# Kernel optimization log

Measured on AMD Instinct MI355X. Metric: run time of the kernel, lower is better.

The kernel has to match this reference:

```python
import jax, jax.numpy as jnp
import numpy as np

N_HEADS = 16
NEG_INF = -1e30  # stand-in for -inf, safe in fp32/bf16


def setup_inputs() -> dict:
    key = jax.random.key(0)
    k1, k2, k3, k4 = jax.random.split(key, 4)
    B, T, C = 8, 1024, 1024
    x = jax.random.normal(k1, (B, T, C), dtype=jnp.float32)
    # torch nn.Linear weight layout: [out_features, in_features]
    w_attn = jax.random.normal(k2, (3 * C, C), dtype=jnp.float32) * 0.02
    w_proj = jax.random.normal(k3, (C, C), dtype=jnp.float32) * 0.02
    b_proj = jax.random.normal(k4, (C,), dtype=jnp.float32) * 0.02
    return {"x": x, "w_attn": w_attn, "w_proj": w_proj, "b_proj": b_proj}


def reference(x, w_attn, w_proj, b_proj):
    B, T, C = x.shape
    H = N_HEADS
    d = C // H
    # fused QKV projection (bias=False); source splits as keys, queries, values
    qkv = x @ w_attn.T  # [B, T, 3C]
    k, q, v = jnp.split(qkv, 3, axis=-1)
    # [B, T, C] -> [B, H, T, d]
    k = k.reshape(B, T, H, d).transpose(0, 2, 1, 3)
    q = q.reshape(B, T, H, d).transpose(0, 2, 1, 3)
    v = v.reshape(B, T, H, d).transpose(0, 2, 1, 3)
    scale = 1.0 / jnp.sqrt(jnp.asarray(d, dtype=x.dtype))
    att = jnp.einsum('bhqd,bhkd->bhqk', q, k) * scale  # [B, H, T, T]
    causal = jnp.tril(jnp.ones((T, T), dtype=bool))
    att = jnp.where(causal, att, NEG_INF)
    att = jax.nn.softmax(att, axis=-1)
    y = jnp.einsum('bhqk,bhkd->bhqd', att, v)  # [B, H, T, d]
    y = y.transpose(0, 2, 1, 3).reshape(B, T, C)
    return y @ w_proj.T + b_proj
```

## Files before the change

### kernel.cpp

```cpp
#include <hip/hip_runtime.h>
#include <stdint.h>

typedef unsigned short u16;
typedef __attribute__((ext_vector_type(8))) short short8;
typedef __attribute__((ext_vector_type(4))) float f32x4;

__device__ __forceinline__ float bf2f(u16 u) {
    union { unsigned u; float f; } x; x.u = ((unsigned)u) << 16; return x.f;
}
__device__ __forceinline__ float bf_lo(unsigned w) {
    union { unsigned u; float f; } x; x.u = w << 16; return x.f;
}
__device__ __forceinline__ float bf_hi(unsigned w) {
    union { unsigned u; float f; } x; x.u = w & 0xffff0000u; return x.f;
}
__device__ __forceinline__ u16 f2bf(float f) {
    union { float f; unsigned u; } x; x.f = f;
    unsigned r = x.u + 0x7fffu + ((x.u >> 16) & 1u);
    return (u16)(r >> 16);
}
__device__ __forceinline__ uint4 cvt8(const float* p) {
    float4 a = *reinterpret_cast<const float4*>(p);
    float4 b = *reinterpret_cast<const float4*>(p + 4);
    uint4 r;
    r.x = (unsigned)f2bf(a.x) | ((unsigned)f2bf(a.y) << 16);
    r.y = (unsigned)f2bf(a.z) | ((unsigned)f2bf(a.w) << 16);
    r.z = (unsigned)f2bf(b.x) | ((unsigned)f2bf(b.y) << 16);
    r.w = (unsigned)f2bf(b.z) | ((unsigned)f2bf(b.w) << 16);
    return r;
}

__device__ __forceinline__ void gl16(const u16* g, u16* l) {
    __builtin_amdgcn_global_load_lds(
        (const __attribute__((address_space(1))) void*)g,
        (__attribute__((address_space(3))) void*)l, 16, 0, 0);
}

__global__ __launch_bounds__(256) void cvt_kernel(const float* __restrict__ in,
                                                  u16* __restrict__ out, int n8) {
    int i = blockIdx.x * 256 + threadIdx.x;
    if (i < n8) *reinterpret_cast<uint4*>(&out[(size_t)i * 8]) = cvt8(&in[(size_t)i * 8]);
}

__global__ __launch_bounds__(256) void cvt3_kernel(const float* __restrict__ a, int na8,
                                                   const float* __restrict__ b, int nb8,
                                                   const float* __restrict__ c, int nc8,
                                                   u16* __restrict__ dst) {
    int i = blockIdx.x * 256 + threadIdx.x;
    const float* src; int off;
    if (i < na8)            { src = a; off = i; }
    else if (i < na8 + nb8) { src = b; off = i - na8; }
    else if (i < na8 + nb8 + nc8) { src = c; off = i - na8 - nb8; }
    else return;
    *reinterpret_cast<uint4*>(&dst[(size_t)i * 8]) = cvt8(&src[(size_t)off * 8]);
}

#define BM 128
#define BN 128
#define BK 32
#define BKA 64

template<bool CF32>
__global__ __launch_bounds__(256) void gemm_bt_a(const u16* __restrict__ A,
                                                 const u16* __restrict__ W,
                                                 void* __restrict__ Cv,
                                                 const float* __restrict__ bias,
                                                 int M, int N, int K, int lda,
                                                 u16* __restrict__ vt) {
    __shared__ __align__(16) u16 As[2][BM * BKA];
    __shared__ __align__(16) u16 Ws[2][BN * BKA];

    const int tid  = threadIdx.x;
    const int lane = tid & 63;
    const int w    = tid >> 6;
    const int wr   = w >> 1;
    const int wc   = w & 1;
    const int quad = lane >> 4;
    const int l16  = lane & 15;

    const int row0 = blockIdx.y * BM;
    const int col0 = blockIdx.x * BN;

    const int srow = w * 8 + (lane >> 3);
    const int gc   = (lane & 7) ^ (lane >> 3);

    const u16* gA[4]; const u16* gW[4];
#pragma unroll
    for (int p = 0; p < 4; p++) {
        gA[p] = A + (size_t)(row0 + p * 32 + srow) * lda + gc * 8;
        gW[p] = W + (size_t)(col0 + p * 32 + srow) * K  + gc * 8;
    }
    const int lofs = (w * 8) * BKA;

    const int cr0 = (quad ^ (l16 & 7)) * 8;

    f32x4 acc[4][4] = {};

#pragma unroll
    for (int p = 0; p < 4; p++) {
        gl16(gA[p], &As[0][p * 32 * BKA + lofs]);
        gl16(gW[p], &Ws[0][p * 32 * BKA + lofs]);
    }

    int cur = 0;
    for (int k0 = 0; k0 < K; k0 += BKA) {
        __syncthreads();
        if (k0 + BKA < K) {
            const int nxt = cur ^ 1;
#pragma unroll
            for (int p = 0; p < 4; p++) {
                gl16(gA[p] + k0 + BKA, &As[nxt][p * 32 * BKA + lofs]);
                gl16(gW[p] + k0 + BKA, &Ws[nxt][p * 32 * BKA + lofs]);
            }
        }

#pragma unroll
        for (int ks = 0; ks < 2; ks++) {
            const int cc = cr0 ^ (ks * 32);
            short8 af[4], bfr[4];
#pragma unroll
            for (int i = 0; i < 4; i++)
                af[i] = *reinterpret_cast<const short8*>(&As[cur][(wr * 64 + i * 16 + l16) * BKA + cc]);
#pragma unroll
            for (int j = 0; j < 4; j++)
                bfr[j] = *reinterpret_cast<const short8*>(&Ws[cur][(wc * 64 + j * 16 + l16) * BKA + cc]);
#pragma unroll
            for (int i = 0; i < 4; i++)
#pragma unroll
                for (int j = 0; j < 4; j++)
                    acc[i][j] = __builtin_amdgcn_mfma_f32_16x16x32_bf16(af[i], bfr[j], acc[i][j], 0, 0, 0);
        }
        cur ^= 1;
    }

    if (vt != nullptr && col0 >= 2048) {
        const int b = row0 >> 10;
#pragma unroll
        for (int j = 0; j < 4; j++) {
            const int hd = col0 - 2048 + wc * 64 + j * 16 + l16;
            u16* dstc = vt + (size_t)(b * 1024 + hd) * 1024 + (row0 & 1023) + wr * 64;
#pragma unroll
            for (int i = 0; i < 4; i++) {
                const int t0 = i * 16 + quad * 4;
                u16 pk[4];
#pragma unroll
                for (int r = 0; r < 4; r++) pk[r] = f2bf(acc[i][j][r]);
                *reinterpret_cast<uint2*>(dstc + t0) = *reinterpret_cast<uint2*>(pk);
            }
        }
    } else {
#pragma unroll
        for (int j = 0; j < 4; j++) {
            const int col = col0 + wc * 64 + j * 16 + l16;
            const float bval = bias ? bias[col] : 0.0f;
#pragma unroll
            for (int i = 0; i < 4; i++) {
#pragma unroll
                for (int r = 0; r < 4; r++) {
                    const int row = row0 + wr * 64 + i * 16 + quad * 4 + r;
                    if (CF32) ((float*)Cv)[(size_t)row * N + col] = acc[i][j][r] + bval;
                    else      ((u16*)Cv)[(size_t)row * N + col]  = f2bf(acc[i][j][r] + bval);
                }
            }
        }
    }
}

template<bool AF32, bool WF32, bool CF32>
__global__ __launch_bounds__(256) void gemm_bt(const void* __restrict__ Av,
                                               const void* __restrict__ Wv,
                                               void* __restrict__ Cv,
                                               const float* __restrict__ bias,
                                               int M, int N, int K, int lda) {
    __shared__ __align__(16) u16 As[BM * BK];
    __shared__ __align__(16) u16 Ws[BN * BK];

    const int tid  = threadIdx.x;
    const int lane = tid & 63;
    const int wave = tid >> 6;
    const int wr   = wave >> 1;
    const int wc   = wave & 1;
    const int quad = lane >> 4;
    const int l16  = lane & 15;

    const int row0 = blockIdx.y * BM;
    const int col0 = blockIdx.x * BN;

    const int sr = tid >> 2;
    const int sc = (tid & 3) * 8;

    f32x4 acc[4][4] = {};

    for (int k0 = 0; k0 < K; k0 += BK) {
        __syncthreads();
        if (AF32) {
            const float* A = (const float*)Av;
            *reinterpret_cast<uint4*>(&As[(sr)      * BK + sc]) = cvt8(&A[(size_t)(row0 + sr)      * lda + k0 + sc]);
            *reinterpret_cast<uint4*>(&As[(sr + 64) * BK + sc]) = cvt8(&A[(size_t)(row0 + sr + 64) * lda + k0 + sc]);
        } else {
            const u16* A = (const u16*)Av;
            *reinterpret_cast<uint4*>(&As[(sr)      * BK + sc]) =
                *reinterpret_cast<const uint4*>(&A[(size_t)(row0 + sr)      * lda + k0 + sc]);
            *reinterpret_cast<uint4*>(&As[(sr + 64) * BK + sc]) =
                *reinterpret_cast<const uint4*>(&A[(size_t)(row0 + sr + 64) * lda + k0 + sc]);
        }
        if (WF32) {
            const float* W = (const float*)Wv;
            *reinterpret_cast<uint4*>(&Ws[(sr)      * BK + sc]) = cvt8(&W[(size_t)(col0 + sr)      * K + k0 + sc]);
            *reinterpret_cast<uint4*>(&Ws[(sr + 64) * BK + sc]) = cvt8(&W[(size_t)(col0 + sr + 64) * K + k0 + sc]);
        } else {
            const u16* W = (const u16*)Wv;
            *reinterpret_cast<uint4*>(&Ws[(sr)      * BK + sc]) =
                *reinterpret_cast<const uint4*>(&W[(size_t)(col0 + sr)      * K + k0 + sc]);
            *reinterpret_cast<uint4*>(&Ws[(sr + 64) * BK + sc]) =
                *reinterpret_cast<const uint4*>(&W[(size_t)(col0 + sr + 64) * K + k0 + sc]);
        }
        __syncthreads();

        short8 af[4], bfr[4];
#pragma unroll
        for (int i = 0; i < 4; i++)
            af[i] = *reinterpret_cast<const short8*>(&As[(wr * 64 + i * 16 + l16) * BK + quad * 8]);
#pragma unroll
        for (int j = 0; j < 4; j++)
            bfr[j] = *reinterpret_cast<const short8*>(&Ws[(wc * 64 + j * 16 + l16) * BK + quad * 8]);

#pragma unroll
        for (int i = 0; i < 4; i++)
#pragma unroll
            for (int j = 0; j < 4; j++)
                acc[i][j] = __builtin_amdgcn_mfma_f32_16x16x32_bf16(af[i], bfr[j], acc[i][j], 0, 0, 0);
    }

#pragma unroll
    for (int j = 0; j < 4; j++) {
        const int col = col0 + wc * 64 + j * 16 + l16;
        const float bval = bias ? bias[col] : 0.0f;
#pragma unroll
        for (int i = 0; i < 4; i++) {
#pragma unroll
            for (int r = 0; r < 4; r++) {
                const int row = row0 + wr * 64 + i * 16 + quad * 4 + r;
                if (CF32) ((float*)Cv)[(size_t)row * N + col] = acc[i][j][r] + bval;
                else      ((u16*)Cv)[(size_t)row * N + col]  = f2bf(acc[i][j][r] + bval);
            }
        }
    }
}

__global__ __launch_bounds__(256) void vtrans_kernel(const u16* __restrict__ qkv,
                                                     u16* __restrict__ vt) {
    const int bid = blockIdx.x;
    const int tt = bid & 15, h = (bid >> 4) & 15, b = bid >> 8;
    const int t0 = tt * 64;
    __shared__ __align__(16) u16 tile[64 * 72];
    const int tr = threadIdx.x >> 2, tc = (threadIdx.x & 3) * 16;
    const u16* src = qkv + (size_t)(b * 1024 + t0 + tr) * 3072 + 2048 + h * 64 + tc;
    *reinterpret_cast<uint4*>(&tile[tr * 72 + tc])     = *reinterpret_cast<const uint4*>(src);
    *reinterpret_cast<uint4*>(&tile[tr * 72 + tc + 8]) = *reinterpret_cast<const uint4*>(src + 8);
    __syncthreads();
    const int dh = tr, t1 = tc;
    __align__(16) u16 buf[16];
#pragma unroll
    for (int i = 0; i < 16; i++) buf[i] = tile[(t1 + i) * 72 + dh];
    u16* dst = vt + ((size_t)(b * 16 + h) * 64 + dh) * 1024 + t0 + t1;
    *reinterpret_cast<uint4*>(dst)     = *reinterpret_cast<uint4*>(&buf[0]);
    *reinterpret_cast<uint4*>(dst + 8) = *reinterpret_cast<uint4*>(&buf[8]);
}

#define SK 72

__global__ __launch_bounds__(256) void fattn_kernel(u16* __restrict__ qkv,
                                                    const u16* __restrict__ vt) {
    __shared__ __align__(16) u16 Ks[64 * SK];
    __shared__ __align__(16) u16 Vs[64 * SK];
    __shared__ __align__(16) u16 Ps[4][32 * SK];
    __shared__ __align__(16) float aS[4][32];

    const int tid  = threadIdx.x;
    const int lane = tid & 63;
    const int w    = tid >> 6;
    const int quad = lane >> 4;
    const int l16  = lane & 15;

    const int bid = blockIdx.x;
    const int qt  = 7 - (bid >> 7);
    const int bh  = bid & 127;
    const int b   = bh >> 4;
    const int h   = bh & 15;

    u16* qb        = qkv + (size_t)b * 1024 * 3072;
    const u16* vtb = vt + (size_t)bh * 64 * 1024;

    const int qrow0 = qt * 128 + w * 32;

    short8 qf[2][2];
#pragma unroll
    for (int mj = 0; mj < 2; mj++)
#pragma unroll
        for (int ks = 0; ks < 2; ks++) {
            const u16* src = qb + (size_t)(qrow0 + mj * 16 + l16) * 3072 + 1024 + h * 64 + ks * 32 + quad * 8;
            __align__(16) u16 tmp[8];
            *reinterpret_cast<uint4*>(tmp) = *reinterpret_cast<const uint4*>(src);
#pragma unroll
            for (int e = 0; e < 8; e++) tmp[e] = f2bf(bf2f(tmp[e]) * 0.125f);
            qf[mj][ks] = *reinterpret_cast<short8*>(tmp);
        }

    f32x4 oa[2][4] = {};
    float m_run[2] = {-1e30f, -1e30f};
    float l_run[2] = {0.f, 0.f};

    const int jtmax = 2 * qt + 1;
    for (int jt = 0; jt <= jtmax; jt++) {
        const int j0 = jt * 64;
        __syncthreads();
        {
            const int sr = tid >> 2, sc = (tid & 3) * 8;
            const u16* kg = qb + (size_t)(j0 + sr) * 3072 + h * 64;
            *reinterpret_cast<uint4*>(&Ks[sr * SK + sc])      = *reinterpret_cast<const uint4*>(kg + sc);
            *reinterpret_cast<uint4*>(&Ks[sr * SK + sc + 32]) = *reinterpret_cast<const uint4*>(kg + sc + 32);
            const u16* vg = vtb + (size_t)sr * 1024 + j0;
            *reinterpret_cast<uint4*>(&Vs[sr * SK + sc])      = *reinterpret_cast<const uint4*>(vg + sc);
            *reinterpret_cast<uint4*>(&Vs[sr * SK + sc + 32]) = *reinterpret_cast<const uint4*>(vg + sc + 32);
        }
        __syncthreads();

        if (j0 > qrow0 + 31) continue;

        f32x4 s[4][2] = {};
#pragma unroll
        for (int ks = 0; ks < 2; ks++) {
            short8 kf[4];
#pragma unroll
            for (int ti = 0; ti < 4; ti++)
                kf[ti] = *reinterpret_cast<const short8*>(&Ks[(ti * 16 + l16) * SK + ks * 32 + quad * 8]);
#pragma unroll
            for (int ti = 0; ti < 4; ti++)
#pragma unroll
                for (int mj = 0; mj < 2; mj++)
                    s[ti][mj] = __builtin_amdgcn_mfma_f32_16x16x32_bf16(kf[ti], qf[mj][ks], s[ti][mj], 0, 0, 0);
        }

        const bool need_mask = (j0 + 63 > qrow0);
#pragma unroll
        for (int mj = 0; mj < 2; mj++) {
            const int mg = qrow0 + mj * 16 + l16;
            if (need_mask) {
#pragma unroll
                for (int ti = 0; ti < 4; ti++)
#pragma unroll
                    for (int r = 0; r < 4; r++)
                        if (j0 + ti * 16 + quad * 4 + r > mg) s[ti][mj][r] = -1e30f;
            }
            float mt = -1e30f;
#pragma unroll
            for (int ti = 0; ti < 4; ti++)
#pragma unroll
                for (int r = 0; r < 4; r++) mt = fmaxf(mt, s[ti][mj][r]);
            mt = fmaxf(mt, __shfl_xor(mt, 16));
            mt = fmaxf(mt, __shfl_xor(mt, 32));
            const float mn    = fmaxf(m_run[mj], mt);
            const float alpha = __expf(m_run[mj] - mn);
            m_run[mj] = mn;
            float ls = 0.f;
#pragma unroll
            for (int ti = 0; ti < 4; ti++)
#pragma unroll
                for (int r = 0; r < 4; r++) {
                    const float p = __expf(s[ti][mj][r] - mn);
                    s[ti][mj][r] = p;
                    ls += p;
                }
            ls += __shfl_xor(ls, 16);
            ls += __shfl_xor(ls, 32);
            l_run[mj] = l_run[mj] * alpha + ls;
            if (lane < 16) aS[w][mj * 16 + l16] = alpha;
#pragma unroll
            for (int ti = 0; ti < 4; ti++) {
                uint2 pk;
                pk.x = (unsigned)f2bf(s[ti][mj][0]) | ((unsigned)f2bf(s[ti][mj][1]) << 16);
                pk.y = (unsigned)f2bf(s[ti][mj][2]) | ((unsigned)f2bf(s[ti][mj][3]) << 16);
                *reinterpret_cast<uint2*>(&Ps[w][(mj * 16 + l16) * SK + ti * 16 + quad * 4]) = pk;
            }
        }

#pragma unroll
        for (int mi = 0; mi < 2; mi++) {
            const f32x4 av = *reinterpret_cast<const f32x4*>(&aS[w][mi * 16 + quad * 4]);
#pragma unroll
            for (int nd = 0; nd < 4; nd++)
#pragma unroll
                for (int r = 0; r < 4; r++) oa[mi][nd][r] *= av[r];
        }

#pragma unroll
        for (int ks = 0; ks < 2; ks++) {
            short8 pf[2], vf[4];
#pragma unroll
            for (int mi = 0; mi < 2; mi++)
                pf[mi] = *reinterpret_cast<const short8*>(&Ps[w][(mi * 16 + l16) * SK + ks * 32 + quad * 8]);
#pragma unroll
            for (int nd = 0; nd < 4; nd++)
                vf[nd] = *reinterpret_cast<const short8*>(&Vs[(nd * 16 + l16) * SK + ks * 32 + quad * 8]);
#pragma unroll
            for (int mi = 0; mi < 2; mi++)
#pragma unroll
                for (int nd = 0; nd < 4; nd++)
                    oa[mi][nd] = __builtin_amdgcn_mfma_f32_16x16x32_bf16(pf[mi], vf[nd], oa[mi][nd], 0, 0, 0);
        }
    }

    if (lane < 16) { aS[w][l16] = 1.f / l_run[0]; aS[w][16 + l16] = 1.f / l_run[1]; }
#pragma unroll
    for (int mi = 0; mi < 2; mi++) {
        const f32x4 iv = *reinterpret_cast<const f32x4*>(&aS[w][mi * 16 + quad * 4]);
#pragma unroll
        for (int nd = 0; nd < 4; nd++)
#pragma unroll
            for (int r = 0; r < 4; r++) {
                const int row = qrow0 + mi * 16 + quad * 4 + r;
                qb[(size_t)row * 3072 + 1024 + h * 64 + nd * 16 + l16] = f2bf(oa[mi][nd][r] * iv[r]);
            }
    }
}

__global__ __launch_bounds__(256) void attn_kernel(u16* __restrict__ qkv) {
    const int g  = blockIdx.x * 256 + threadIdx.x;
    const int q  = g & 1023;
    const int bh = g >> 10;
    const int b  = bh >> 4;
    const int h  = bh & 15;
    const size_t base = (size_t)b * 1024 * 3072 + (size_t)h * 64;
    float qv[64];
    {
        const uint4* q4 = reinterpret_cast<const uint4*>(qkv + base + (size_t)q * 3072 + 1024);
#pragma unroll
        for (int c = 0; c < 8; c++) {
            uint4 t = q4[c];
            qv[c*8+0]=bf_lo(t.x); qv[c*8+1]=bf_hi(t.x); qv[c*8+2]=bf_lo(t.y); qv[c*8+3]=bf_hi(t.y);
            qv[c*8+4]=bf_lo(t.z); qv[c*8+5]=bf_hi(t.z); qv[c*8+6]=bf_lo(t.w); qv[c*8+7]=bf_hi(t.w);
        }
    }
    float o[64];
#pragma unroll
    for (int i = 0; i < 64; i++) o[i] = 0.0f;
    float m = -1e30f, l = 0.0f;
    const int jmax = q | 63;
    for (int j = 0; j <= jmax; j++) {
        const uint4* k4 = reinterpret_cast<const uint4*>(qkv + base + (size_t)j * 3072);
        float s = 0.0f;
#pragma unroll
        for (int c = 0; c < 8; c++) {
            uint4 t = k4[c];
            s += qv[c*8+0]*bf_lo(t.x)+qv[c*8+1]*bf_hi(t.x)+qv[c*8+2]*bf_lo(t.y)+qv[c*8+3]*bf_hi(t.y)
               + qv[c*8+4]*bf_lo(t.z)+qv[c*8+5]*bf_hi(t.z)+qv[c*8+6]*bf_lo(t.w)+qv[c*8+7]*bf_hi(t.w);
        }
        s *= 0.125f;
        const bool act = (j <= q);
        if (!act) s = -1e30f;
        const float mn = fmaxf(m, s);
        const float alpha = __expf(m - mn);
        float p = __expf(s - mn);
        if (!act) p = 0.0f;
        l = l * alpha + p;
        const uint4* v4 = reinterpret_cast<const uint4*>(qkv + base + (size_t)j * 3072 + 2048);
#pragma unroll
        for (int c = 0; c < 8; c++) {
            uint4 t = v4[c];
            o[c*8+0]=o[c*8+0]*alpha+p*bf_lo(t.x); o[c*8+1]=o[c*8+1]*alpha+p*bf_hi(t.x);
            o[c*8+2]=o[c*8+2]*alpha+p*bf_lo(t.y); o[c*8+3]=o[c*8+3]*alpha+p*bf_hi(t.y);
            o[c*8+4]=o[c*8+4]*alpha+p*bf_lo(t.z); o[c*8+5]=o[c*8+5]*alpha+p*bf_hi(t.z);
            o[c*8+6]=o[c*8+6]*alpha+p*bf_lo(t.w); o[c*8+7]=o[c*8+7]*alpha+p*bf_hi(t.w);
        }
        m = mn;
    }
    const float inv = 1.0f / l;
    u16* yrow = qkv + base + (size_t)q * 3072 + 1024;
#pragma unroll
    for (int i = 0; i < 64; i++) yrow[i] = f2bf(o[i] * inv);
}

extern "C" void kernel_launch(void* const* d_in, const int* in_sizes, int n_in,
                              void* d_out, int out_size, void* d_ws, size_t ws_size,
                              hipStream_t stream) {
    const float* x      = (const float*)d_in[0];
    const float* w_attn = (const float*)d_in[1];
    const float* w_proj = (const float*)d_in[2];
    const float* b_proj = (const float*)d_in[3];
    float* out = (float*)d_out;

    const int M = 8192, K = 1024;
    const size_t QKV = (size_t)8192 * 3072;
    const size_t VT  = (size_t)8 * 16 * 64 * 1024;

    u16* qkv = (u16*)d_ws;
    u16* vtb = qkv + QKV;
    u16* xb  = vtb + VT;
    u16* wab = xb + (size_t)8192 * 1024;
    u16* wpb = wab + (size_t)3072 * 1024;

    const size_t need_full = (QKV + VT + (size_t)8192*1024 + (size_t)3072*1024 + (size_t)1024*1024) * 2;
    const size_t need_mid  = (QKV + VT) * 2;

    if (ws_size >= need_full) {
        cvt3_kernel<<<6144, 256, 0, stream>>>(x, 8192 * 1024 / 8,
                                              w_attn, 3072 * 1024 / 8,
                                              w_proj, 1024 * 1024 / 8, xb);
        gemm_bt_a<false><<<dim3(24, 64), 256, 0, stream>>>(xb, wab, qkv, nullptr, M, 3072, K, K, vtb);
        fattn_kernel<<<1024, 256, 0, stream>>>(qkv, vtb);
        gemm_bt_a<true><<<dim3(8, 64), 256, 0, stream>>>(qkv + 1024, wpb, out, b_proj, M, 1024, K, 3072, nullptr);
    } else if (ws_size >= need_mid) {
        gemm_bt<true, true, false><<<dim3(24, 64), 256, 0, stream>>>(x, w_attn, qkv, nullptr, M, 3072, K, K);
        vtrans_kernel<<<2048, 256, 0, stream>>>(qkv, vtb);
        fattn_kernel<<<1024, 256, 0, stream>>>(qkv, vtb);
        gemm_bt<false, true, true><<<dim3(8, 64), 256, 0, stream>>>(qkv + 1024, w_proj, out, b_proj, M, 1024, K, 3072);
    } else {
        gemm_bt<true, true, false><<<dim3(24, 64), 256, 0, stream>>>(x, w_attn, qkv, nullptr, M, 3072, K, K);
        attn_kernel<<<512, 256, 0, stream>>>(qkv);
        gemm_bt<false, true, true><<<dim3(8, 64), 256, 0, stream>>>(qkv + 1024, w_proj, out, b_proj, M, 1024, K, 3072);
    }
}
```

Measured before the change: 234.7 us.

## Use direct global-to-LDS loads in attention, single-buffer GEMM tiles

```diff
diff --git a/kernel.cpp b/kernel.cpp
--- a/kernel.cpp
+++ b/kernel.cpp
@@ -67,8 +67,8 @@
                                                  const float* __restrict__ bias,
                                                  int M, int N, int K, int lda,
                                                  u16* __restrict__ vt) {
-    __shared__ __align__(16) u16 As[2][BM * BKA];
-    __shared__ __align__(16) u16 Ws[2][BN * BKA];
+    __shared__ __align__(16) u16 As[BM * BKA];
+    __shared__ __align__(16) u16 Ws[BN * BKA];
 
     const int tid  = threadIdx.x;
     const int lane = tid & 63;
@@ -84,35 +84,27 @@
     const int srow = w * 8 + (lane >> 3);
     const int gc   = (lane & 7) ^ (lane >> 3);
 
-    const u16* gA[4]; const u16* gW[4];
+    const u16* gA[4]; const u16* gW[4]; u16* lA[4]; u16* lW[4];
 #pragma unroll
     for (int p = 0; p < 4; p++) {
         gA[p] = A + (size_t)(row0 + p * 32 + srow) * lda + gc * 8;
         gW[p] = W + (size_t)(col0 + p * 32 + srow) * K  + gc * 8;
-    }
-    const int lofs = (w * 8) * BKA;
+        lA[p] = &As[(p * 32 + w * 8) * BKA];
+        lW[p] = &Ws[(p * 32 + w * 8) * BKA];
+    }
 
     const int cr0 = (quad ^ (l16 & 7)) * 8;
 
     f32x4 acc[4][4] = {};
 
-#pragma unroll
-    for (int p = 0; p < 4; p++) {
-        gl16(gA[p], &As[0][p * 32 * BKA + lofs]);
-        gl16(gW[p], &Ws[0][p * 32 * BKA + lofs]);
-    }
-
-    int cur = 0;
     for (int k0 = 0; k0 < K; k0 += BKA) {
         __syncthreads();
-        if (k0 + BKA < K) {
-            const int nxt = cur ^ 1;
-#pragma unroll
-            for (int p = 0; p < 4; p++) {
-                gl16(gA[p] + k0 + BKA, &As[nxt][p * 32 * BKA + lofs]);
-                gl16(gW[p] + k0 + BKA, &Ws[nxt][p * 32 * BKA + lofs]);
-            }
-        }
+#pragma unroll
+        for (int p = 0; p < 4; p++) {
+            gl16(gA[p] + k0, lA[p]);
+            gl16(gW[p] + k0, lW[p]);
+        }
+        __syncthreads();
 
 #pragma unroll
         for (int ks = 0; ks < 2; ks++) {
@@ -120,17 +112,16 @@
             short8 af[4], bfr[4];
 #pragma unroll
             for (int i = 0; i < 4; i++)
-                af[i] = *reinterpret_cast<const short8*>(&As[cur][(wr * 64 + i * 16 + l16) * BKA + cc]);
+                af[i] = *reinterpret_cast<const short8*>(&As[(wr * 64 + i * 16 + l16) * BKA + cc]);
 #pragma unroll
             for (int j = 0; j < 4; j++)
-                bfr[j] = *reinterpret_cast<const short8*>(&Ws[cur][(wc * 64 + j * 16 + l16) * BKA + cc]);
+                bfr[j] = *reinterpret_cast<const short8*>(&Ws[(wc * 64 + j * 16 + l16) * BKA + cc]);
 #pragma unroll
             for (int i = 0; i < 4; i++)
 #pragma unroll
                 for (int j = 0; j < 4; j++)
                     acc[i][j] = __builtin_amdgcn_mfma_f32_16x16x32_bf16(af[i], bfr[j], acc[i][j], 0, 0, 0);
         }
-        cur ^= 1;
     }
 
     if (vt != nullptr && col0 >= 2048) {
@@ -272,8 +263,8 @@
 
 __global__ __launch_bounds__(256) void fattn_kernel(u16* __restrict__ qkv,
                                                     const u16* __restrict__ vt) {
-    __shared__ __align__(16) u16 Ks[64 * SK];
-    __shared__ __align__(16) u16 Vs[64 * SK];
+    __shared__ __align__(16) u16 Ks[64 * 64];
+    __shared__ __align__(16) u16 Vs[64 * 64];
     __shared__ __align__(16) u16 Ps[4][32 * SK];
     __shared__ __align__(16) float aS[4][32];
 
@@ -294,6 +285,9 @@
 
     const int qrow0 = qt * 128 + w * 32;
 
+    const int srow8 = lane >> 3;
+    const int scg   = (lane & 7) ^ srow8;
+
     short8 qf[2][2];
 #pragma unroll
     for (int mj = 0; mj < 2; mj++)
@@ -315,14 +309,11 @@
     for (int jt = 0; jt <= jtmax; jt++) {
         const int j0 = jt * 64;
         __syncthreads();
-        {
-            const int sr = tid >> 2, sc = (tid & 3) * 8;
-            const u16* kg = qb + (size_t)(j0 + sr) * 3072 + h * 64;
-            *reinterpret_cast<uint4*>(&Ks[sr * SK + sc])      = *reinterpret_cast<const uint4*>(kg + sc);
-            *reinterpret_cast<uint4*>(&Ks[sr * SK + sc + 32]) = *reinterpret_cast<const uint4*>(kg + sc + 32);
-            const u16* vg = vtb + (size_t)sr * 1024 + j0;
-            *reinterpret_cast<uint4*>(&Vs[sr * SK + sc])      = *reinterpret_cast<const uint4*>(vg + sc);
-            *reinterpret_cast<uint4*>(&Vs[sr * SK + sc + 32]) = *reinterpret_cast<const uint4*>(vg + sc + 32);
+#pragma unroll
+        for (int p = 0; p < 2; p++) {
+            const int r = w * 16 + p * 8 + srow8;
+            gl16(qb + (size_t)(j0 + r) * 3072 + h * 64 + scg * 8, &Ks[(w * 16 + p * 8) * 64]);
+            gl16(vtb + (size_t)r * 1024 + j0 + scg * 8,           &Vs[(w * 16 + p * 8) * 64]);
         }
         __syncthreads();
 
@@ -334,7 +325,8 @@
             short8 kf[4];
 #pragma unroll
             for (int ti = 0; ti < 4; ti++)
-                kf[ti] = *reinterpret_cast<const short8*>(&Ks[(ti * 16 + l16) * SK + ks * 32 + quad * 8]);
+                kf[ti] = *reinterpret_cast<const short8*>(
+                    &Ks[(ti * 16 + l16) * 64 + (((ks * 4 + quad) ^ (l16 & 7)) * 8)]);
 #pragma unroll
             for (int ti = 0; ti < 4; ti++)
 #pragma unroll
@@ -402,7 +394,8 @@
                 pf[mi] = *reinterpret_cast<const short8*>(&Ps[w][(mi * 16 + l16) * SK + ks * 32 + quad * 8]);
 #pragma unroll
             for (int nd = 0; nd < 4; nd++)
-                vf[nd] = *reinterpret_cast<const short8*>(&Vs[(nd * 16 + l16) * SK + ks * 32 + quad * 8]);
+                vf[nd] = *reinterpret_cast<const short8*>(
+                    &Vs[(nd * 16 + l16) * 64 + (((ks * 4 + quad) ^ (l16 & 7)) * 8)]);
 #pragma unroll
             for (int mi = 0; mi < 2; mi++)
 #pragma unroll
```

After: 240.3 us. +2.4%, slower.
